# Kernel optimization log

Measured on AMD Instinct MI355X. Metric: run time of the kernel, lower is better.

The kernel has to match this reference:

```python
import jax, jax.numpy as jnp
import numpy as np

B, C, N, K, COUT = 8, 128, 10000, 16, 256


def setup_inputs() -> dict:
    key = jax.random.key(0)
    ks = jax.random.split(key, 8)
    x = jax.random.normal(ks[0], (B, C, N, 1), dtype=jnp.float32)
    edge_index = jax.random.randint(ks[1], (2, B, N, K), 0, N)
    s1 = 1.0 / np.sqrt(C)
    W1 = jax.random.uniform(ks[2], (C, C), jnp.float32, -s1, s1)   # nn1 1x1 conv weight
    b1 = jax.random.uniform(ks[3], (C,), jnp.float32, -s1, s1)
    Wp = jax.random.uniform(ks[4], (C, C), jnp.float32, -s1, s1)   # nn_pooling Linear
    bp = jax.random.uniform(ks[5], (C,), jnp.float32, -s1, s1)
    s2 = 1.0 / np.sqrt(2 * C)
    W2 = jax.random.uniform(ks[6], (COUT, 2 * C), jnp.float32, -s2, s2)  # nn2 1x1 conv
    b2 = jax.random.uniform(ks[7], (COUT,), jnp.float32, -s2, s2)
    return dict(x=x, edge_index=edge_index, W1=W1, b1=b1, Wp=Wp, bp=bp, W2=W2, b2=b2)


def reference(x, edge_index, W1, b1, Wp, bp, W2, b2):
    b, c, n, _ = x.shape
    k = edge_index.shape[-1]
    # nn1: 1x1 conv (channel mix) + ReLU -> [B,C,N,1]
    h = jax.nn.relu(jnp.einsum('bcns,dc->bdns', x, W1) + b1[None, :, None, None])
    # batched_index_select: gather neighbor features along vertex dim -> [B,C,N,K]
    hn = h[:, :, :, 0]                              # [B,C,N]
    idx = edge_index[0].reshape(b, 1, n * k)        # broadcast over C
    xj = jnp.take_along_axis(hn, idx, axis=2).reshape(b, c, n, k)
    # nn_pooling: Linear over channel dim + ReLU (transpose(1,3) in torch == act on C)
    xj = jax.nn.relu(jnp.einsum('bcnk,dc->bdnk', xj, Wp) + bp[None, :, None, None])
    # max-pool over neighbors, keepdim -> [B,C,N,1]
    xj = jnp.max(xj, axis=-1, keepdims=True)
    # concat along channels, nn2: 1x1 conv + ReLU -> [B,COUT,N,1]
    cat = jnp.concatenate([h, xj], axis=1)
    out = jax.nn.relu(jnp.einsum('bcns,dc->bdns', cat, W2) + b2[None, :, None, None])
    return out
```

## Files before the change

kernel.cpp:

```cpp
#include <hip/hip_runtime.h>

#define NODES 10000
#define BATCH 8
#define CH    128
#define KNB   16
#define CO    256

typedef __bf16 bf16x8 __attribute__((ext_vector_type(8)));
typedef float  f32x4  __attribute__((ext_vector_type(4)));

__device__ __forceinline__ unsigned short f2bf(float f) {
  unsigned u = __float_as_uint(f);
  u = (u + 0x7FFFu + ((u >> 16) & 1u)) >> 16;
  return (unsigned short)u;
}
__device__ __forceinline__ unsigned pk2(float a, float b) {
  return (unsigned)f2bf(a) | ((unsigned)f2bf(b) << 16);
}
__device__ __forceinline__ unsigned pkmax(unsigned a, unsigned b) {
  unsigned d;
  asm("v_pk_max_u16 %0, %1, %2" : "=v"(d) : "v"(a), "v"(b));
  return d;
}
__device__ __forceinline__ uint4 pkmax4(uint4 a, uint4 b) {
  a.x = pkmax(a.x, b.x); a.y = pkmax(a.y, b.y);
  a.z = pkmax(a.z, b.z); a.w = pkmax(a.w, b.w);
  return a;
}
__device__ __forceinline__ bf16x8 asbf8(uint4 u) {
  union { uint4 u; bf16x8 b; } c; c.u = u; return c.b;
}

__global__ __launch_bounds__(256) void prep(
    const float* __restrict__ W1, const float* __restrict__ Wp,
    const float* __restrict__ W2,
    unsigned short* __restrict__ W1b, unsigned short* __restrict__ Wpb,
    unsigned short* __restrict__ W2b)
{
  int i = blockIdx.x * 256 + threadIdx.x;
  const float* src; unsigned short* dst; int off;
  if (i < 4096)      { src = W1; dst = W1b; off = i; }
  else if (i < 8192) { src = Wp; dst = Wpb; off = i - 4096; }
  else               { src = W2; dst = W2b; off = i - 8192; }
  float4 v = ((const float4*)src)[off];
  ushort4 o;
  o.x = f2bf(v.x); o.y = f2bf(v.y); o.z = f2bf(v.z); o.w = f2bf(v.w);
  ((ushort4*)dst)[off] = o;
}

__global__ __launch_bounds__(256) void fused_hz(
    const unsigned short* __restrict__ W1b, const float* __restrict__ b1,
    const unsigned short* __restrict__ Wpb, const float* __restrict__ bp,
    const float* __restrict__ x,
    unsigned short* __restrict__ h_t, unsigned short* __restrict__ z_t)
{
  const int b    = blockIdx.y;
  const int t    = threadIdx.x;
  const int w    = t >> 6, lane = t & 63;
  const int lm   = lane & 15, q = lane >> 4;
  const int nw0  = blockIdx.x * 128 + w * 32;

  __shared__ __align__(16) unsigned short Hs_all[4][32 * 128];
  char* Hs = (char*)Hs_all[w];

  int node[2], gn[2];
  node[0] = nw0 + lm;      gn[0] = node[0] < NODES ? node[0] : NODES - 1;
  node[1] = nw0 + 16 + lm; gn[1] = node[1] < NODES ? node[1] : NODES - 1;

  uint4 B1[2][4];
#pragma unroll
  for (int nt = 0; nt < 2; ++nt) {
    const float* X = x + (size_t)b * CH * NODES + gn[nt];
    float xv[32];
#pragma unroll
    for (int kt = 0; kt < 4; ++kt)
#pragma unroll
      for (int j = 0; j < 8; ++j)
        xv[kt * 8 + j] = X[(size_t)(kt * 32 + q * 8 + j) * NODES];
#pragma unroll
    for (int kt = 0; kt < 4; ++kt) {
      B1[nt][kt].x = pk2(xv[kt * 8 + 0], xv[kt * 8 + 1]);
      B1[nt][kt].y = pk2(xv[kt * 8 + 2], xv[kt * 8 + 3]);
      B1[nt][kt].z = pk2(xv[kt * 8 + 4], xv[kt * 8 + 5]);
      B1[nt][kt].w = pk2(xv[kt * 8 + 6], xv[kt * 8 + 7]);
    }
  }

  uint4 a[2][4];
#pragma unroll
  for (int kt = 0; kt < 4; ++kt) {
    a[0][kt] = *(const uint4*)(W1b + (size_t)(lm) * CH + kt * 32 + q * 8);
    a[1][kt] = *(const uint4*)(W1b + (size_t)(16 + lm) * CH + kt * 32 + q * 8);
  }
#pragma unroll
  for (int dt = 0; dt < 8; ++dt) {
    f32x4 acc0 = (f32x4){0.f, 0.f, 0.f, 0.f};
    f32x4 acc1 = (f32x4){0.f, 0.f, 0.f, 0.f};
#pragma unroll
    for (int kt = 0; kt < 4; ++kt) {
      acc0 = __builtin_amdgcn_mfma_f32_16x16x32_bf16(
          asbf8(a[dt & 1][kt]), asbf8(B1[0][kt]), acc0, 0, 0, 0);
      acc1 = __builtin_amdgcn_mfma_f32_16x16x32_bf16(
          asbf8(a[dt & 1][kt]), asbf8(B1[1][kt]), acc1, 0, 0, 0);
    }
    if (dt < 6) {
#pragma unroll
      for (int kt = 0; kt < 4; ++kt)
        a[dt & 1][kt] = *(const uint4*)(W1b + (size_t)((dt + 2) * 16 + lm) * CH
                                        + kt * 32 + q * 8);
    }
    const int d0 = dt * 16 + q * 4;
    float4 bi = *(const float4*)(b1 + d0);
    f32x4 aa[2] = {acc0, acc1};
#pragma unroll
    for (int nt = 0; nt < 2; ++nt) {
      ushort4 o;
      o.x = f2bf(fmaxf(aa[nt][0] + bi.x, 0.f));
      o.y = f2bf(fmaxf(aa[nt][1] + bi.y, 0.f));
      o.z = f2bf(fmaxf(aa[nt][2] + bi.z, 0.f));
      o.w = f2bf(fmaxf(aa[nt][3] + bi.w, 0.f));
      const int row = nt * 16 + lm;
      const int chunk = dt * 2 + (q >> 1);
      *(ushort4*)(Hs + row * 256 + ((chunk ^ (row & 7)) << 4) + ((q & 1) << 3)) = o;
    }
  }

  uint4 B2[2][4];
#pragma unroll
  for (int nt = 0; nt < 2; ++nt) {
    const int row = nt * 16 + lm;
#pragma unroll
    for (int kt = 0; kt < 4; ++kt)
      B2[nt][kt] = *(const uint4*)(Hs + row * 256 + (((kt * 4 + q) ^ (row & 7)) << 4));
  }

  {
    const int srow = lane >> 4, schk = lane & 15;
#pragma unroll
    for (int p = 0; p < 8; ++p) {
      const int row = p * 4 + srow;
      const int gnode = nw0 + row;
      uint4 vv = *(const uint4*)(Hs + row * 256 + ((schk ^ (row & 7)) << 4));
      if (gnode < NODES)
        *(uint4*)(h_t + ((size_t)b * NODES + gnode) * CH + schk * 8) = vv;
    }
  }

#pragma unroll
  for (int kt = 0; kt < 4; ++kt) {
    a[0][kt] = *(const uint4*)(Wpb + (size_t)(lm) * CH + kt * 32 + q * 8);
    a[1][kt] = *(const uint4*)(Wpb + (size_t)(16 + lm) * CH + kt * 32 + q * 8);
  }
#pragma unroll
  for (int dt = 0; dt < 8; ++dt) {
    f32x4 acc0 = (f32x4){0.f, 0.f, 0.f, 0.f};
    f32x4 acc1 = (f32x4){0.f, 0.f, 0.f, 0.f};
#pragma unroll
    for (int kt = 0; kt < 4; ++kt) {
      acc0 = __builtin_amdgcn_mfma_f32_16x16x32_bf16(
          asbf8(a[dt & 1][kt]), asbf8(B2[0][kt]), acc0, 0, 0, 0);
      acc1 = __builtin_amdgcn_mfma_f32_16x16x32_bf16(
          asbf8(a[dt & 1][kt]), asbf8(B2[1][kt]), acc1, 0, 0, 0);
    }
    if (dt < 6) {
#pragma unroll
      for (int kt = 0; kt < 4; ++kt)
        a[dt & 1][kt] = *(const uint4*)(Wpb + (size_t)((dt + 2) * 16 + lm) * CH
                                        + kt * 32 + q * 8);
    }
    const int d0 = dt * 16 + q * 4;
    float4 bi = *(const float4*)(bp + d0);
    f32x4 aa[2] = {acc0, acc1};
#pragma unroll
    for (int nt = 0; nt < 2; ++nt) {
      ushort4 o;
      o.x = f2bf(fmaxf(aa[nt][0] + bi.x, 0.f));
      o.y = f2bf(fmaxf(aa[nt][1] + bi.y, 0.f));
      o.z = f2bf(fmaxf(aa[nt][2] + bi.z, 0.f));
      o.w = f2bf(fmaxf(aa[nt][3] + bi.w, 0.f));
      const int row = nt * 16 + lm;
      const int chunk = dt * 2 + (q >> 1);
      *(ushort4*)(Hs + row * 256 + ((chunk ^ (row & 7)) << 4) + ((q & 1) << 3)) = o;
    }
  }

  {
    const int srow = lane >> 4, schk = lane & 15;
#pragma unroll
    for (int p = 0; p < 8; ++p) {
      const int row = p * 4 + srow;
      const int gnode = nw0 + row;
      uint4 vv = *(const uint4*)(Hs + row * 256 + ((schk ^ (row & 7)) << 4));
      if (gnode < NODES)
        *(uint4*)(z_t + ((size_t)b * NODES + gnode) * CH + schk * 8) = vv;
    }
  }
}

__global__ __launch_bounds__(256) void out_kernel(
    const unsigned short* __restrict__ h_t, const unsigned short* __restrict__ z_t,
    const int* __restrict__ e0, const unsigned short* __restrict__ W2b,
    const float* __restrict__ b2, float* __restrict__ out)
{
  const int bid = blockIdx.x;
  const int b   = bid & 7;
  const int n0  = (bid >> 3) * 64;
  const int t   = threadIdx.x;
  const int lane = t & 63, w = t >> 6;
  const int lm = lane & 15, q = lane >> 4;

  __shared__ __align__(16) unsigned short cat[64 * 256];
  char* catB = (char*)cat;

  {
    const int nl = t >> 2, c = t & 3;
    int gn = n0 + nl; if (gn >= NODES) gn = NODES - 1;

    const int* ep = e0 + ((size_t)b * NODES + gn) * KNB;
    uint4 iv0 = *(const uint4*)(ep);
    uint4 iv1 = *(const uint4*)(ep + 4);
    uint4 iv2 = *(const uint4*)(ep + 8);
    uint4 iv3 = *(const uint4*)(ep + 12);
    unsigned jns[KNB] = {iv0.x, iv0.y, iv0.z, iv0.w, iv1.x, iv1.y, iv1.z, iv1.w,
                         iv2.x, iv2.y, iv2.z, iv2.w, iv3.x, iv3.y, iv3.z, iv3.w};

    const unsigned short* H = h_t + ((size_t)b * NODES + gn) * CH;
#pragma unroll
    for (int j = 0; j < 4; ++j) {
      const int ch = 4 * j + c;
      uint4 hv = *(const uint4*)(H + ch * 8);
      *(uint4*)(catB + nl * 512 + ((ch ^ (nl & 7)) << 4)) = hv;
    }

    const unsigned short* Zb = z_t + (size_t)b * NODES * CH;
#pragma unroll
    for (int cg = 0; cg < 4; ++cg) {
      const int ch = cg * 4 + c;
      uint4 v[KNB];
#pragma unroll
      for (int k = 0; k < KNB; ++k)
        v[k] = *(const uint4*)(Zb + (size_t)jns[k] * CH + ch * 8);
#pragma unroll
      for (int k = 0; k < 8; ++k) v[k] = pkmax4(v[k], v[k + 8]);
#pragma unroll
      for (int k = 0; k < 4; ++k) v[k] = pkmax4(v[k], v[k + 4]);
      v[0] = pkmax4(v[0], v[2]);
      v[1] = pkmax4(v[1], v[3]);
      v[0] = pkmax4(v[0], v[1]);
      *(uint4*)(catB + nl * 512 + (((16 + ch) ^ (nl & 7)) << 4)) = v[0];
    }
  }

  __syncthreads();

  const int d0 = w * 64;
  f32x4 acc[4][4];
#pragma unroll
  for (int dt = 0; dt < 4; ++dt)
#pragma unroll
    for (int nt = 0; nt < 4; ++nt) acc[dt][nt] = (f32x4){0.f, 0.f, 0.f, 0.f};

  uint4 acur[4], anxt[4];
#pragma unroll
  for (int dt = 0; dt < 4; ++dt)
    acur[dt] = *(const uint4*)(W2b + (size_t)(d0 + dt * 16 + lm) * CO + q * 8);

#pragma unroll
  for (int kt = 0; kt < 8; ++kt) {
    if (kt < 7) {
#pragma unroll
      for (int dt = 0; dt < 4; ++dt)
        anxt[dt] = *(const uint4*)(W2b + (size_t)(d0 + dt * 16 + lm) * CO
                                   + (kt + 1) * 32 + q * 8);
    }
#pragma unroll
    for (int nt = 0; nt < 4; ++nt) {
      const int nl = nt * 16 + lm;
      const int chunk = kt * 4 + q;
      bf16x8 bb = asbf8(*(const uint4*)(catB + nl * 512 + ((chunk ^ (nl & 7)) << 4)));
#pragma unroll
      for (int dt = 0; dt < 4; ++dt)
        acc[dt][nt] = __builtin_amdgcn_mfma_f32_16x16x32_bf16(
            asbf8(acur[dt]), bb, acc[dt][nt], 0, 0, 0);
    }
#pragma unroll
    for (int dt = 0; dt < 4; ++dt) acur[dt] = anxt[dt];
  }

#pragma unroll
  for (int dt = 0; dt < 4; ++dt) {
    const int dbase = d0 + dt * 16 + q * 4;
    float4 bi = *(const float4*)(b2 + dbase);
    float bv[4] = {bi.x, bi.y, bi.z, bi.w};
#pragma unroll
    for (int nt = 0; nt < 4; ++nt) {
      const int gn = n0 + nt * 16 + lm;
      if (gn < NODES) {
        float* op = out + (size_t)(b * CO + dbase) * NODES + gn;
#pragma unroll
        for (int r = 0; r < 4; ++r)
          op[(size_t)r * NODES] = fmaxf(acc[dt][nt][r] + bv[r], 0.f);
      }
    }
  }
}

extern "C" void kernel_launch(void* const* d_in, const int* in_sizes, int n_in,
                              void* d_out, int out_size, void* d_ws, size_t ws_size,
                              hipStream_t stream) {
  const float* x  = (const float*)d_in[0];
  const int*   ei = (const int*)d_in[1];
  const float* W1 = (const float*)d_in[2];
  const float* b1 = (const float*)d_in[3];
  const float* Wp = (const float*)d_in[4];
  const float* bp = (const float*)d_in[5];
  const float* W2 = (const float*)d_in[6];
  const float* b2 = (const float*)d_in[7];
  float* out = (float*)d_out;

  unsigned short* ws  = (unsigned short*)d_ws;
  unsigned short* h_t = ws;
  unsigned short* z_t = h_t + (size_t)BATCH * NODES * CH;
  unsigned short* W1b = z_t + (size_t)BATCH * NODES * CH;
  unsigned short* Wpb = W1b + CH * CH;
  unsigned short* W2b = Wpb + CH * CH;

  prep<<<96, 256, 0, stream>>>(W1, Wp, W2, W1b, Wpb, W2b);

  const int NTF = (NODES + 127) / 128;
  fused_hz<<<dim3(NTF, BATCH), 256, 0, stream>>>(W1b, b1, Wpb, bp, x, h_t, z_t);

  const int NTO = (NODES + 63) / 64;
  out_kernel<<<BATCH * NTO, 256, 0, stream>>>(h_t, z_t, ei, W2b, b2, out);
}
```

Baseline: 205.3 us.

## Split neighbor gather-max into a separate kernel before the output GEMM

Moves the 16-neighbor gather and packed bf16 max out of the output GEMM kernel into a standalone gather_max kernel. Each wave now handles 4 nodes with 16 lanes per node covering all channels, and writes the pooled features to a new workspace buffer. The GEMM kernel then only loads h and the pooled features with coalesced reads before its MFMA loop. The aim is to let the latency-bound random gather run at high occupancy without holding up the GEMM. The cost is an extra launch plus a write and re-read of a B*N*C bf16 intermediate.

```diff
diff --git a/kernel.cpp b/kernel.cpp
--- a/kernel.cpp
+++ b/kernel.cpp
@@ -197,10 +197,50 @@
   }
 }
 
-__global__ __launch_bounds__(256) void out_kernel(
-    const unsigned short* __restrict__ h_t, const unsigned short* __restrict__ z_t,
-    const int* __restrict__ e0, const unsigned short* __restrict__ W2b,
-    const float* __restrict__ b2, float* __restrict__ out)
+__global__ __launch_bounds__(256) void gather_max(
+    const unsigned short* __restrict__ z_t, const int* __restrict__ e0,
+    unsigned short* __restrict__ xj_t)
+{
+  const int bid = blockIdx.x;
+  const int b   = bid & 7;
+  const int n0  = (bid >> 3) * 16;
+  const int t   = threadIdx.x;
+  const int wv  = t >> 6, lane = t & 63;
+  const int r   = lane >> 4, c16 = lane & 15;
+
+  const int n  = n0 + wv * 4 + r;
+  const int gn = (n < NODES) ? n : (NODES - 1);
+
+  const int* ep = e0 + ((size_t)b * NODES + gn) * KNB;
+  uint4 i0 = *(const uint4*)(ep);
+  uint4 i1 = *(const uint4*)(ep + 4);
+  uint4 i2 = *(const uint4*)(ep + 8);
+  uint4 i3 = *(const uint4*)(ep + 12);
+  unsigned jns[KNB] = {i0.x, i0.y, i0.z, i0.w, i1.x, i1.y, i1.z, i1.w,
+                       i2.x, i2.y, i2.z, i2.w, i3.x, i3.y, i3.z, i3.w};
+
+  const unsigned short* Zb = z_t + (size_t)b * NODES * CH;
+  uint4 v[KNB];
+#pragma unroll
+  for (int k = 0; k < KNB; ++k)
+    v[k] = *(const uint4*)(Zb + (size_t)jns[k] * CH + c16 * 8);
+
+#pragma unroll
+  for (int k = 0; k < 8; ++k) v[k] = pkmax4(v[k], v[k + 8]);
+#pragma unroll
+  for (int k = 0; k < 4; ++k) v[k] = pkmax4(v[k], v[k + 4]);
+  v[0] = pkmax4(v[0], v[2]);
+  v[1] = pkmax4(v[1], v[3]);
+  v[0] = pkmax4(v[0], v[1]);
+
+  if (n < NODES)
+    *(uint4*)(xj_t + ((size_t)b * NODES + n) * CH + c16 * 8) = v[0];
+}
+
+__global__ __launch_bounds__(256) void out_gemm(
+    const unsigned short* __restrict__ h_t, const unsigned short* __restrict__ xj_t,
+    const unsigned short* __restrict__ W2b, const float* __restrict__ b2,
+    float* __restrict__ out)
 {
   const int bid = blockIdx.x;
   const int b   = bid & 7;
@@ -213,41 +253,15 @@
   char* catB = (char*)cat;
 
   {
-    const int nl = t >> 2, c = t & 3;
-    int gn = n0 + nl; if (gn >= NODES) gn = NODES - 1;
-
-    const int* ep = e0 + ((size_t)b * NODES + gn) * KNB;
-    uint4 iv0 = *(const uint4*)(ep);
-    uint4 iv1 = *(const uint4*)(ep + 4);
-    uint4 iv2 = *(const uint4*)(ep + 8);
-    uint4 iv3 = *(const uint4*)(ep + 12);
-    unsigned jns[KNB] = {iv0.x, iv0.y, iv0.z, iv0.w, iv1.x, iv1.y, iv1.z, iv1.w,
-                         iv2.x, iv2.y, iv2.z, iv2.w, iv3.x, iv3.y, iv3.z, iv3.w};
-
-    const unsigned short* H = h_t + ((size_t)b * NODES + gn) * CH;
-#pragma unroll
-    for (int j = 0; j < 4; ++j) {
-      const int ch = 4 * j + c;
-      uint4 hv = *(const uint4*)(H + ch * 8);
-      *(uint4*)(catB + nl * 512 + ((ch ^ (nl & 7)) << 4)) = hv;
-    }
-
-    const unsigned short* Zb = z_t + (size_t)b * NODES * CH;
-#pragma unroll
-    for (int cg = 0; cg < 4; ++cg) {
-      const int ch = cg * 4 + c;
-      uint4 v[KNB];
-#pragma unroll
-      for (int k = 0; k < KNB; ++k)
-        v[k] = *(const uint4*)(Zb + (size_t)jns[k] * CH + ch * 8);
-#pragma unroll
-      for (int k = 0; k < 8; ++k) v[k] = pkmax4(v[k], v[k + 8]);
-#pragma unroll
-      for (int k = 0; k < 4; ++k) v[k] = pkmax4(v[k], v[k + 4]);
-      v[0] = pkmax4(v[0], v[2]);
-      v[1] = pkmax4(v[1], v[3]);
-      v[0] = pkmax4(v[0], v[1]);
-      *(uint4*)(catB + nl * 512 + (((16 + ch) ^ (nl & 7)) << 4)) = v[0];
+    const int nl = t >> 4, c16 = t & 15;
+#pragma unroll
+    for (int rep = 0; rep < 4; ++rep) {
+      const int row = rep * 16 + nl;
+      const int gn = (n0 + row < NODES) ? (n0 + row) : (NODES - 1);
+      uint4 hv = *(const uint4*)(h_t + ((size_t)b * NODES + gn) * CH + c16 * 8);
+      *(uint4*)(catB + row * 512 + ((c16 ^ (row & 7)) << 4)) = hv;
+      uint4 xv = *(const uint4*)(xj_t + ((size_t)b * NODES + gn) * CH + c16 * 8);
+      *(uint4*)(catB + row * 512 + (((16 + c16) ^ (row & 7)) << 4)) = xv;
     }
   }
 
@@ -318,18 +332,22 @@
   const float* b2 = (const float*)d_in[7];
   float* out = (float*)d_out;
 
-  unsigned short* ws  = (unsigned short*)d_ws;
-  unsigned short* h_t = ws;
-  unsigned short* z_t = h_t + (size_t)BATCH * NODES * CH;
-  unsigned short* W1b = z_t + (size_t)BATCH * NODES * CH;
-  unsigned short* Wpb = W1b + CH * CH;
-  unsigned short* W2b = Wpb + CH * CH;
+  unsigned short* ws   = (unsigned short*)d_ws;
+  unsigned short* h_t  = ws;
+  unsigned short* z_t  = h_t  + (size_t)BATCH * NODES * CH;
+  unsigned short* xj_t = z_t  + (size_t)BATCH * NODES * CH;
+  unsigned short* W1b  = xj_t + (size_t)BATCH * NODES * CH;
+  unsigned short* Wpb  = W1b + CH * CH;
+  unsigned short* W2b  = Wpb + CH * CH;
 
   prep<<<96, 256, 0, stream>>>(W1, Wp, W2, W1b, Wpb, W2b);
 
   const int NTF = (NODES + 127) / 128;
   fused_hz<<<dim3(NTF, BATCH), 256, 0, stream>>>(W1b, b1, Wpb, bp, x, h_t, z_t);
 
+  const int NTG = (NODES + 15) / 16;
+  gather_max<<<BATCH * NTG, 256, 0, stream>>>(z_t, ei, xj_t);
+
   const int NTO = (NODES + 63) / 64;
-  out_kernel<<<BATCH * NTO, 256, 0, stream>>>(h_t, z_t, ei, W2b, b2, out);
-}
+  out_gemm<<<BATCH * NTO, 256, 0, stream>>>(h_t, xj_t, W2b, b2, out);
+}
```

After: 206.0 us. Within noise of the previous version (+0.3%).
